# Kernel tuning notes

Measured on AMD Instinct MI355X. Metric: run time of the kernel, lower is better.

The kernel has to match this reference:

```python
import jax, jax.numpy as jnp
import numpy as np


def _lstm(x, h, c, Wih, Whh, b):
    # torch.nn.LSTMCell gate order: input, forget, cell(g), output
    g = x @ Wih + h @ Whh + b
    i, f, gg, o = jnp.split(g, 4, axis=-1)
    c = jax.nn.sigmoid(f) * c + jax.nn.sigmoid(i) * jnp.tanh(gg)
    h = jax.nn.sigmoid(o) * jnp.tanh(c)
    return h, c


def _forward(memory, mel_target, memory_lengths, prenet_W1, prenet_W2, query_W,
             memory_W, weight_vec, loc_conv_W, loc_dense_W, att_Wih, att_Whh, att_b,
             dec_Wih, dec_Whh, dec_b, proj_W, proj_b, gate_W, gate_b):
    B, n_mels, T_mel = mel_target.shape
    T_enc, enc_dim = memory.shape[1], memory.shape[2]
    att_rnn, dec_rnn = att_Whh.shape[0], dec_Whh.shape[0]
    # decoder inputs: zero frame + teacher-forced mels, one per step -> [T_mel, B, n_mels]
    dec_in = jnp.concatenate(
        [jnp.zeros((1, B, n_mels), memory.dtype), jnp.transpose(mel_target, (2, 0, 1))], 0)[:T_mel]
    # PreNet (dropout disabled: eval mode, torch uses train=self.training)
    pre = jax.nn.relu(jax.nn.relu(dec_in @ prenet_W1) @ prenet_W2)  # [T_mel, B, 256]
    processed_memory = memory @ memory_W                             # [B, T_enc, att_dim]
    valid = jnp.arange(T_enc)[None, :] < memory_lengths[:, None]     # [B, T_enc]
    pad = (loc_conv_W.shape[-1] - 1) // 2

    def step(carry, p):
        ah, ac, dh, dc, aw, awc, ctx = carry
        # attention RNN
        ah, ac = _lstm(jnp.concatenate([p, ctx], -1), ah, ac, att_Wih, att_Whh, att_b)
        # location features: conv over [prev_weights, cum_weights]
        awcat = jnp.stack([aw, awc], 1)                              # [B, 2, T_enc]
        loc = jax.lax.conv_general_dilated(awcat, loc_conv_W, (1,), [(pad, pad)],
                                           dimension_numbers=('NCH', 'OIH', 'NCH'))
        loc = jnp.einsum('bft,fa->bta', loc, loc_dense_W)            # [B, T_enc, att_dim]
        # energies and attention
        q = ah @ query_W                                             # [B, att_dim]
        e = jnp.einsum('bta,a->bt', jnp.tanh(q[:, None, :] + processed_memory + loc), weight_vec)
        e = jnp.where(valid, e, -jnp.inf)
        aw = jax.nn.softmax(e, axis=-1)                              # [B, T_enc]
        ctx = jnp.einsum('bt,btd->bd', aw, memory)                   # [B, enc_dim]
        awc = awc + aw
        # decoder RNN + projections
        dh, dc = _lstm(jnp.concatenate([ah, ctx], -1), dh, dc, dec_Wih, dec_Whh, dec_b)
        do = jnp.concatenate([dh, ctx], -1)
        mel = do @ proj_W + proj_b                                   # [B, n_mels]
        gate = (do @ gate_W + gate_b)[:, 0]                          # [B]
        return (ah, ac, dh, dc, aw, awc, ctx), (mel, gate, aw)

    z = lambda d: jnp.zeros((B, d), memory.dtype)
    carry0 = (z(att_rnn), z(att_rnn), z(dec_rnn), z(dec_rnn),
              jnp.zeros((B, T_enc), memory.dtype), jnp.zeros((B, T_enc), memory.dtype), z(enc_dim))
    _, (mels, gates, aligns) = jax.lax.scan(jax.checkpoint(step), carry0, pre)
    return (jnp.transpose(mels, (1, 2, 0)),   # [B, n_mels, T_mel]
            jnp.transpose(gates, (1, 0)),     # [B, T_mel]
            jnp.transpose(aligns, (1, 0, 2)))  # [B, T_mel, T_enc]


def setup_inputs() -> dict:
    key = jax.random.key(0)
    ks = jax.random.split(key, 20)
    B, T_enc, T_mel = 32, 400, 400
    n_mels, pre, att_rnn, dec_rnn, enc_dim, att_dim, nf, ksz = 80, 256, 1024, 1024, 512, 128, 32, 31
    rn = lambda k, s, sc=0.02: (jax.random.normal(k, s, jnp.float32) * sc)
    return dict(
        memory=jax.random.normal(ks[0], (B, T_enc, enc_dim), jnp.float32),
        mel_target=jax.random.normal(ks[1], (B, n_mels, T_mel), jnp.float32),
        memory_lengths=jax.random.randint(ks[2], (B,), T_enc // 2, T_enc + 1),
        prenet_W1=rn(ks[3], (n_mels, pre), 0.05),
        prenet_W2=rn(ks[4], (pre, pre), 0.05),
        query_W=rn(ks[5], (att_rnn, att_dim)),
        memory_W=rn(ks[6], (enc_dim, att_dim)),
        weight_vec=rn(ks[7], (att_dim,), 0.1),
        loc_conv_W=rn(ks[8], (nf, 2, ksz), 0.1),
        loc_dense_W=rn(ks[9], (nf, att_dim), 0.1),
        att_Wih=rn(ks[10], (pre + enc_dim, 4 * att_rnn)),
        att_Whh=rn(ks[11], (att_rnn, 4 * att_rnn)),
        att_b=jnp.zeros((4 * att_rnn,), jnp.float32),
        dec_Wih=rn(ks[12], (att_rnn + enc_dim, 4 * dec_rnn)),
        dec_Whh=rn(ks[13], (dec_rnn, 4 * dec_rnn)),
        dec_b=jnp.zeros((4 * dec_rnn,), jnp.float32),
        proj_W=rn(ks[14], (dec_rnn + enc_dim, n_mels)),
        proj_b=jnp.zeros((n_mels,), jnp.float32),
        gate_W=rn(ks[15], (dec_rnn + enc_dim, 1)),
        gate_b=jnp.zeros((1,), jnp.float32),
    )


def reference(memory, mel_target, memory_lengths, prenet_W1, prenet_W2, query_W,
              memory_W, weight_vec, loc_conv_W, loc_dense_W, att_Wih, att_Whh, att_b,
              dec_Wih, dec_Whh, dec_b, proj_W, proj_b, gate_W, gate_b):
    return _forward(memory, mel_target, memory_lengths, prenet_W1, prenet_W2, query_W,
                    memory_W, weight_vec, loc_conv_W, loc_dense_W, att_Wih, att_Whh, att_b,
                    dec_Wih, dec_Whh, dec_b, proj_W, proj_b, gate_W, gate_b)
```

## Files before the change

kernel.cpp:

```cpp
#include <hip/hip_runtime.h>

#define OFF_PRE   0u
#define OFF_PMT   3276800u
#define OFF_GATT  4915200u
#define OFF_GDEC  7012352u
#define OFF_E     9109504u
#define OFF_AH    9122304u
#define OFF_AC0   9155072u
#define OFF_AC1   9187840u
#define OFF_DH    9220608u
#define OFF_DC    9253376u
#define OFF_AW0   9286144u
#define OFF_AW1   9298944u
#define OFF_AWC0  9311744u
#define OFF_AWC1  9324544u
#define OFF_CTX0  9337344u
#define OFF_CTX1  9353728u
#define WS_TOTAL  9370112u

__device__ __forceinline__ float sigm(float x){ return 1.f/(1.f+__expf(-x)); }
__device__ __forceinline__ float ftanh(float x){
  x = fminf(fmaxf(x,-15.f),15.f);
  float e = __expf(2.f*x);
  return (e-1.f)/(e+1.f);
}

typedef const __attribute__((address_space(1))) unsigned int* gas_t;
typedef __attribute__((address_space(3))) unsigned int* las_t;


__global__ void zero_kernel(float* p, unsigned n){
  unsigned i = blockIdx.x*256u + threadIdx.x;
  if (i<n) p[i]=0.f;
}

__global__ __launch_bounds__(256) void prenet_kernel(const float* __restrict__ mel_target,
    const float* __restrict__ W1, const float* __restrict__ W2, float* __restrict__ pre)
{
  __shared__ float din[80];
  __shared__ float h1[256];
  int blk = blockIdx.x;
  int t = blk >> 5, b = blk & 31;
  int tid = threadIdx.x;
  if (tid < 80) din[tid] = (t==0) ? 0.f : mel_target[b*32000 + tid*400 + (t-1)];
  __syncthreads();
  float s=0.f;
  for (int c=0;c<80;c++) s += din[c]*W1[c*256+tid];
  h1[tid] = fmaxf(s,0.f);
  __syncthreads();
  float s2=0.f;
  for (int c=0;c<256;c++) s2 += h1[c]*W2[c*256+tid];
  pre[(size_t)blk*256 + tid] = fmaxf(s2,0.f);
}

__global__ __launch_bounds__(128) void pm_kernel(const float* __restrict__ memory,
    const float* __restrict__ memory_W, float* __restrict__ pmT)
{
  __shared__ float mrow[512];
  int blk = blockIdx.x;
  int b = blk/400, t = blk - b*400;
  int tid = threadIdx.x;
  const float* src = memory + (size_t)blk*512;
  for (int i=tid;i<512;i+=128) mrow[i]=src[i];
  __syncthreads();
  float s=0.f;
  for (int d=0; d<512; d++) s += mrow[d]*memory_W[d*128+tid];
  pmT[(size_t)b*51200 + tid*400 + t] = s;
}

template<int SLICE, int KIH>
__global__ __launch_bounds__(512) void gates_v3(
    const float* __restrict__ x0, int n0,
    const float* __restrict__ x1, int n1,
    const float* __restrict__ x2, int n2,
    const float* __restrict__ Wih, const float* __restrict__ Whh,
    float* __restrict__ Gp)
{
  constexpr int NT = SLICE/16;
  __shared__ float xs[SLICE*33];
  __shared__ float wbuf[3*2048];
  const int tid = threadIdx.x;
  const int k_beg = blockIdx.y * SLICE;
  const int n01 = n0 + n1;

  for (int base=0; base<32*SLICE; base+=512){
    int idx = base + tid;
    if (idx < 32*SLICE){
      int r = idx / SLICE, kk = idx - r*SLICE;
      int k = k_beg + kk;
      float v;
      if (k < n0) v = x0[r*n0 + k];
      else if (k < n01) v = x1[r*n1 + (k-n0)];
      else v = x2[r*n2 + (k-n01)];
      xs[kk*33 + r] = v;
    }
  }
  __syncthreads();

  const int wv = tid >> 6, lane = tid & 63;
  const int fb = wv*1024 + lane*16;
  const int kk_l = fb >> 9;
  const int inner = fb & 511;
  const size_t colbB = (size_t)blockIdx.x*512;

  auto STAGE = [&](int s){
    int k = k_beg + s*16 + kk_l;
    const char* row = (k < KIH) ? ((const char*)Wih + (size_t)k*16384)
                                : ((const char*)Whh + (size_t)(k-KIH)*16384);
    const char* g = row + colbB + inner;
    float* l = &wbuf[(s%3)*2048 + wv*256];
    __builtin_amdgcn_global_load_lds((gas_t)g, (las_t)l, 16, 0, 0);
  };

  STAGE(0);
  STAGE(1);

  const int rg = tid >> 5, cg = tid & 31;
  const int r0 = rg*2;
  float4 a0 = {0,0,0,0}, a1 = {0,0,0,0};

  for (int s=0; s<NT; s++){
    asm volatile("s_barrier" ::: "memory");
    if (s+2 < NT) STAGE(s+2);
    int rem = NT-1-s;
    if (rem >= 2)      asm volatile("s_waitcnt vmcnt(2)" ::: "memory");
    else if (rem == 1) asm volatile("s_waitcnt vmcnt(1)" ::: "memory");
    else               asm volatile("s_waitcnt vmcnt(0)" ::: "memory");
    asm volatile("s_barrier" ::: "memory");
    const float* wb = &wbuf[(s%3)*2048];
    const float* xk = &xs[(s*16)*33];
    #pragma unroll
    for (int kk=0; kk<16; kk++){
      float4 w = *(const float4*)(wb + kk*128 + cg*4);
      float xv0 = xk[kk*33 + r0], xv1 = xk[kk*33 + r0 + 1];
      a0.x += xv0*w.x; a0.y += xv0*w.y; a0.z += xv0*w.z; a0.w += xv0*w.w;
      a1.x += xv1*w.x; a1.y += xv1*w.y; a1.z += xv1*w.z; a1.w += xv1*w.w;
    }
  }
  float* gp = Gp + (size_t)blockIdx.y*131072 + blockIdx.x*128 + cg*4;
  *(float4*)(gp + (size_t)(r0  )*4096) = a0;
  *(float4*)(gp + (size_t)(r0+1)*4096) = a1;
}

__global__ __launch_bounds__(512) void att_mid_kernel(
    const float* __restrict__ Gp, const float* __restrict__ att_b,
    float* __restrict__ AH, const float* __restrict__ ACr, float* __restrict__ ACw,
    const float* __restrict__ query_W,
    const float* __restrict__ wc, const float* __restrict__ wd,
    const float* __restrict__ vvec, const float* __restrict__ pmT,
    const int* __restrict__ mlen,
    const float* __restrict__ AWr, const float* __restrict__ AWCr,
    float* __restrict__ E,
    const float* __restrict__ Gd, const float* __restrict__ dec_b,
    float* __restrict__ DH, float* __restrict__ DC,
    int step)
{
  __shared__ float aw_s[400], awc_s[400];
  __shared__ float wc_s[1984];
  __shared__ float wd_s[4096];
  __shared__ float v_s[128], q_s[128];
  __shared__ float ah_s[1024];
  __shared__ float pool[4608];
  const int b = blockIdx.x, yD = blockIdx.y, tid = threadIdx.x;

  for (int i=tid;i<400;i+=512){ aw_s[i]=AWr[b*400+i]; awc_s[i]=AWCr[b*400+i]; }
  for (int i=tid;i<4096;i+=512) wd_s[i]=wd[i];
  for (int i=tid;i<1984;i+=512) wc_s[i]=wc[i];
  if (tid<128) v_s[tid]=vvec[tid];

  {
    float4* g4 = (float4*)pool;
    for (int i=tid; i<1024; i+=512){
      float4 s = {0,0,0,0};
      #pragma unroll
      for (int sl=0; sl<16; sl++){
        const float4* gs = (const float4*)(Gp + (size_t)sl*131072 + (size_t)b*4096);
        float4 v = gs[i];
        s.x+=v.x; s.y+=v.y; s.z+=v.z; s.w+=v.w;
      }
      g4[i] = s;
    }
  }
  __syncthreads();
  for (int u0=0; u0<2; u0++){
    int u = tid + u0*512;
    float gi=pool[u]+att_b[u], gf=pool[1024+u]+att_b[1024+u];
    float gg=pool[2048+u]+att_b[2048+u], go=pool[3072+u]+att_b[3072+u];
    float c = sigm(gf)*ACr[b*1024+u] + sigm(gi)*ftanh(gg);
    float h = sigm(go)*ftanh(c);
    ah_s[u]=h;
    if (yD==0){ ACw[b*1024+u]=c; AH[b*1024+u]=h; }
  }
  __syncthreads();
  { int a = tid & 127, sl = tid >> 7;
    float s=0.f; int kb = sl*256;
    for (int k=kb;k<kb+256;k++) s += ah_s[k]*query_W[k*128+a];
    pool[sl*128+a]=s; }
  __syncthreads();
  if (tid<128) q_s[tid] = pool[tid]+pool[128+tid]+pool[256+tid]+pool[384+tid];
  if (step>0 && tid<128){
    int u = yD*128 + tid;
    float gi=dec_b[u], gf=dec_b[1024+u], gg=dec_b[2048+u], go=dec_b[3072+u];
    #pragma unroll
    for (int sl=0; sl<16; sl++){
      const float* g = Gd + (size_t)sl*131072 + (size_t)b*4096;
      gi+=g[u]; gf+=g[1024+u]; gg+=g[2048+u]; go+=g[3072+u];
    }
    float c = sigm(gf)*DC[b*1024+u] + sigm(gi)*ftanh(gg);
    float h = sigm(go)*ftanh(c);
    DC[b*1024+u]=c; DH[b*1024+u]=h;
  }
  __syncthreads();
  const int t0 = yD*50;
  float* loc = pool + 512;
  { int tl = tid & 63, fs = tid >> 6;
    if (tl < 50){
      float cf0=0,cf1=0,cf2=0,cf3=0;
      int f0 = fs*4;
      int tg = t0 + tl;
      for (int k=0;k<31;k++){
        int gi2 = tg + k - 15;
        float a1 = (gi2>=0 && gi2<400) ? aw_s[gi2] : 0.f;
        float a2 = (gi2>=0 && gi2<400) ? awc_s[gi2] : 0.f;
        cf0 += wc_s[(f0+0)*62+k]*a1 + wc_s[(f0+0)*62+31+k]*a2;
        cf1 += wc_s[(f0+1)*62+k]*a1 + wc_s[(f0+1)*62+31+k]*a2;
        cf2 += wc_s[(f0+2)*62+k]*a1 + wc_s[(f0+2)*62+31+k]*a2;
        cf3 += wc_s[(f0+3)*62+k]*a1 + wc_s[(f0+3)*62+31+k]*a2;
      }
      loc[tl*33+f0+0]=cf0; loc[tl*33+f0+1]=cf1;
      loc[tl*33+f0+2]=cf2; loc[tl*33+f0+3]=cf3;
    }
  }
  __syncthreads();
  float* ep = pool + 2176;
  { int tl = tid & 63, as = tid >> 6;
    if (tl < 50){
      int tg = t0 + tl;
      float e = 0.f;
      const float* lrow = loc + tl*33;
      for (int aa=0; aa<16; aa++){
        int a = as*16 + aa;
        float pmv = pmT[(size_t)b*51200 + (size_t)a*400 + tg];
        float lv = 0.f;
        #pragma unroll
        for (int f=0; f<32; f++) lv += lrow[f]*wd_s[f*128+a];
        e += ftanh(q_s[a]+pmv+lv)*v_s[a];
      }
      ep[as*64+tl] = e;
    }
  }
  __syncthreads();
  if (tid < 50){
    int tg = t0 + tid;
    float ee=0.f;
    #pragma unroll
    for (int as2=0; as2<8; as2++) ee += ep[as2*64+tid];
    E[b*400+tg] = (tg < mlen[b]) ? ee : -1e30f;
  }
}

__global__ __launch_bounds__(512) void softmax_ctx_kernel(
    const float* __restrict__ E, const float* __restrict__ memory,
    float* __restrict__ AWw, const float* __restrict__ AWCr, float* __restrict__ AWCw,
    float* __restrict__ CTXw, const float* __restrict__ CTXpp,
    const float* __restrict__ DH,
    const float* __restrict__ proj_W, const float* __restrict__ proj_b,
    const float* __restrict__ gate_W, const float* __restrict__ gate_b,
    float* __restrict__ out, float* __restrict__ aligns, int step)
{
  __shared__ float e_s[400];
  __shared__ float red[16];
  __shared__ float cp[512];
  __shared__ float do_s[1536];
  __shared__ float pps[486];
  const int b = blockIdx.x, yD = blockIdx.y, tid = threadIdx.x;

  float ev = (tid<400) ? E[b*400+tid] : -1e30f;
  float m = ev;
  for (int off=32; off>0; off>>=1) m = fmaxf(m, __shfl_down(m, off, 64));
  if ((tid&63)==0) red[tid>>6]=m;
  __syncthreads();
  if (tid==0){ float mm=red[0]; for (int i=1;i<8;i++) mm=fmaxf(mm,red[i]); red[8]=mm; }
  __syncthreads();
  m = red[8];
  float ex = (tid<400) ? __expf(ev-m) : 0.f;
  float ss = ex;
  for (int off=32; off>0; off>>=1) ss += __shfl_down(ss, off, 64);
  if ((tid&63)==0) red[tid>>6]=ss;
  __syncthreads();
  if (tid==0){ float s2=0.f; for (int i=0;i<8;i++) s2+=red[i]; red[9]=1.f/s2; }
  __syncthreads();
  float anew = ex*red[9];
  if (tid<400) e_s[tid]=anew;
  if (yD==0 && tid<400){
    AWw[b*400+tid] = anew;
    AWCw[b*400+tid] = AWCr[b*400+tid] + anew;
    aligns[(size_t)b*160000 + (size_t)step*400 + tid] = anew;
  }
  __syncthreads();
  { int d = tid & 63, ts = tid >> 6;
    const int d0 = yD*64;
    const float* mrow = memory + (size_t)b*204800 + d0 + d;
    float pacc=0.f;
    for (int tt=ts*50; tt<ts*50+50; tt++) pacc += e_s[tt]*mrow[(size_t)tt*512];
    cp[ts*64+d]=pacc; }
  __syncthreads();
  if (tid<64){
    float s2=0.f;
    #pragma unroll
    for (int ts2=0; ts2<8; ts2++) s2+=cp[ts2*64+tid];
    CTXw[b*512 + yD*64 + tid]=s2;
  }
  if (yD==0 && step>0){
    for (int i=tid; i<1536; i+=512)
      do_s[i] = (i<1024) ? DH[b*1024+i] : CTXpp[b*512 + (i-1024)];
    __syncthreads();
    int sl = tid/81, o = tid - sl*81;
    if (sl < 6){
      float s=0.f; int kb = sl*256;
      for (int k=kb;k<kb+256;k++){
        float w2 = (o<80) ? proj_W[k*80+o] : gate_W[k];
        s += do_s[k]*w2;
      }
      pps[sl*81+o]=s;
    }
    __syncthreads();
    if (tid<81){
      float r=0.f;
      #pragma unroll
      for (int s2=0;s2<6;s2++) r += pps[s2*81+tid];
      if (tid<80) out[(size_t)b*32000 + tid*400 + (step-1)] = r + proj_b[tid];
      else        out[1024000 + b*400 + (step-1)] = r + gate_b[0];
    }
  }
}

__global__ __launch_bounds__(512) void dec_final_kernel(
    const float* __restrict__ Gd, const float* __restrict__ dec_b,
    const float* __restrict__ DC, const float* __restrict__ CTX1,
    const float* __restrict__ proj_W, const float* __restrict__ proj_b,
    const float* __restrict__ gate_W, const float* __restrict__ gate_b,
    float* __restrict__ out)
{
  __shared__ float g_s[4096];
  __shared__ float do_s[1536];
  __shared__ float pps[486];
  const int b = blockIdx.x, tid = threadIdx.x;
  { float4* g4 = (float4*)g_s;
    for (int i=tid; i<1024; i+=512){
      float4 s={0,0,0,0};
      #pragma unroll
      for (int sl=0; sl<16; sl++){
        const float4* gs = (const float4*)(Gd + (size_t)sl*131072 + (size_t)b*4096);
        float4 v = gs[i];
        s.x+=v.x; s.y+=v.y; s.z+=v.z; s.w+=v.w;
      }
      g4[i]=s;
    } }
  __syncthreads();
  for (int u0=0; u0<2; u0++){
    int u = tid + u0*512;
    float gi=g_s[u]+dec_b[u], gf=g_s[1024+u]+dec_b[1024+u];
    float gg=g_s[2048+u]+dec_b[2048+u], go=g_s[3072+u]+dec_b[3072+u];
    float c = sigm(gf)*DC[b*1024+u] + sigm(gi)*ftanh(gg);
    do_s[u] = sigm(go)*ftanh(c);
  }
  if (tid<512) do_s[1024+tid] = CTX1[b*512+tid];
  __syncthreads();
  int sl = tid/81, o = tid - sl*81;
  if (sl < 6){
    float s=0.f; int kb = sl*256;
    for (int k=kb;k<kb+256;k++){
      float w2 = (o<80) ? proj_W[k*80+o] : gate_W[k];
      s += do_s[k]*w2;
    }
    pps[sl*81+o]=s;
  }
  __syncthreads();
  if (tid<81){
    float r=0.f;
    #pragma unroll
    for (int s2=0;s2<6;s2++) r += pps[s2*81+tid];
    if (tid<80) out[(size_t)b*32000 + tid*400 + 399] = r + proj_b[tid];
    else        out[1024000 + b*400 + 399] = r + gate_b[0];
  }
}


extern "C" void kernel_launch(void* const* d_in, const int* in_sizes, int n_in,
                              void* d_out, int out_size, void* d_ws, size_t ws_size,
                              hipStream_t stream) {
  const float* memory      = (const float*)d_in[0];
  const float* mel_target  = (const float*)d_in[1];
  const int*   mlen        = (const int*)  d_in[2];
  const float* prenet_W1   = (const float*)d_in[3];
  const float* prenet_W2   = (const float*)d_in[4];
  const float* query_W     = (const float*)d_in[5];
  const float* memory_W    = (const float*)d_in[6];
  const float* weight_vec  = (const float*)d_in[7];
  const float* loc_conv_W  = (const float*)d_in[8];
  const float* loc_dense_W = (const float*)d_in[9];
  const float* att_Wih     = (const float*)d_in[10];
  const float* att_Whh     = (const float*)d_in[11];
  const float* att_b       = (const float*)d_in[12];
  const float* dec_Wih     = (const float*)d_in[13];
  const float* dec_Whh     = (const float*)d_in[14];
  const float* dec_b       = (const float*)d_in[15];
  const float* proj_W      = (const float*)d_in[16];
  const float* proj_b      = (const float*)d_in[17];
  const float* gate_W      = (const float*)d_in[18];
  const float* gate_b      = (const float*)d_in[19];
  float* out = (float*)d_out;
  float* ws  = (float*)d_ws;

  float* PRE  = ws + OFF_PRE;
  float* PMT  = ws + OFF_PMT;
  float* GATT = ws + OFF_GATT;
  float* GDEC = ws + OFF_GDEC;
  float* E    = ws + OFF_E;
  float* AH   = ws + OFF_AH;
  float* AC[2] = { ws + OFF_AC0, ws + OFF_AC1 };
  float* DH   = ws + OFF_DH;
  float* DC   = ws + OFF_DC;
  float* AW[2] = { ws + OFF_AW0, ws + OFF_AW1 };
  float* AWC[2]= { ws + OFF_AWC0, ws + OFF_AWC1 };
  float* CTX[2]= { ws + OFF_CTX0, ws + OFF_CTX1 };
  float* aligns = out + 1036800;

  hipLaunchKernelGGL(zero_kernel, dim3((WS_TOTAL+255u)/256u), dim3(256), 0, stream, ws, WS_TOTAL);
  hipLaunchKernelGGL(prenet_kernel, dim3(12800), dim3(256), 0, stream,
                     mel_target, prenet_W1, prenet_W2, PRE);
  hipLaunchKernelGGL(pm_kernel, dim3(12800), dim3(128), 0, stream, memory, memory_W, PMT);

  for (int t=0; t<400; t++){
    const int p = t & 1, pp = 1 - p;
    hipLaunchKernelGGL((gates_v3<112,768>), dim3(32,16), dim3(512), 0, stream,
        PRE + (size_t)t*8192, 256, CTX[pp], 512, AH, 1024,
        att_Wih, att_Whh, GATT);
    hipLaunchKernelGGL(att_mid_kernel, dim3(32,8), dim3(512), 0, stream,
        GATT, att_b, AH, AC[pp], AC[p], query_W, loc_conv_W, loc_dense_W,
        weight_vec, PMT, mlen, AW[pp], AWC[pp], E,
        GDEC, dec_b, DH, DC, t);
    hipLaunchKernelGGL(softmax_ctx_kernel, dim3(32,8), dim3(512), 0, stream,
        E, memory, AW[p], AWC[pp], AWC[p], CTX[p], CTX[pp],
        DH, proj_W, proj_b, gate_W, gate_b, out, aligns, t);
    hipLaunchKernelGGL((gates_v3<160,1536>), dim3(32,16), dim3(512), 0, stream,
        AH, 1024, CTX[p], 512, DH, 1024,
        dec_Wih, dec_Whh, GDEC);
  }
  hipLaunchKernelGGL(dec_final_kernel, dim3(32), dim3(512), 0, stream,
      GDEC, dec_b, DC, CTX[1], proj_W, proj_b, gate_W, gate_b, out);
}
```

Before: 71.90 ms.

## Fuse per-step decoder kernels into one persistent cooperative kernel with grid barriers

Replaces the 1600 per-step kernel launches with a single cooperative persistent kernel of 256 blocks that runs all 400 decoder steps, separating phases with an atomic-counter grid barrier. The gates matmul split-K count drops from 16 to 8 slices (larger slices), so the partial-sum buffers and reductions shrink. Weight staging in the gates phase moves from triple to double buffering, and x loads become float2. This removes launch overhead and inter-kernel gaps but adds spin-barrier costs and reduces parallelism per phase.

```diff
diff --git a/kernel.cpp b/kernel.cpp
--- a/kernel.cpp
+++ b/kernel.cpp
@@ -1,22 +1,28 @@
 #include <hip/hip_runtime.h>
+
+#define NBLK 256
+#define NTHR 512
 
 #define OFF_PRE   0u
 #define OFF_PMT   3276800u
 #define OFF_GATT  4915200u
-#define OFF_GDEC  7012352u
-#define OFF_E     9109504u
-#define OFF_AH    9122304u
-#define OFF_AC0   9155072u
-#define OFF_AC1   9187840u
-#define OFF_DH    9220608u
-#define OFF_DC    9253376u
-#define OFF_AW0   9286144u
-#define OFF_AW1   9298944u
-#define OFF_AWC0  9311744u
-#define OFF_AWC1  9324544u
-#define OFF_CTX0  9337344u
-#define OFF_CTX1  9353728u
-#define WS_TOTAL  9370112u
+#define OFF_GDEC  5963776u
+#define OFF_E     7012352u
+#define OFF_AH    7025152u
+#define OFF_AC0   7057920u
+#define OFF_AC1   7090688u
+#define OFF_DH    7123456u
+#define OFF_DC    7156224u
+#define OFF_AW0   7188992u
+#define OFF_AW1   7201792u
+#define OFF_AWC0  7214592u
+#define OFF_AWC1  7227392u
+#define OFF_CTX0  7240192u
+#define OFF_CTX1  7256576u
+#define OFF_BAR   7272960u
+#define WS_TOTAL  7272976u
+
+#define LDS_FLOATS 14976
 
 __device__ __forceinline__ float sigm(float x){ return 1.f/(1.f+__expf(-x)); }
 __device__ __forceinline__ float ftanh(float x){
@@ -27,6 +33,24 @@
 
 typedef const __attribute__((address_space(1))) unsigned int* gas_t;
 typedef __attribute__((address_space(3))) unsigned int* las_t;
+
+__device__ __forceinline__ void gsync(unsigned* bar){
+  __syncthreads();
+  if (threadIdx.x==0){
+    __threadfence();
+    unsigned g = __hip_atomic_load(bar+1, __ATOMIC_ACQUIRE, __HIP_MEMORY_SCOPE_AGENT);
+    unsigned arrived = __hip_atomic_fetch_add(bar, 1u, __ATOMIC_ACQ_REL, __HIP_MEMORY_SCOPE_AGENT);
+    if (arrived == NBLK-1u){
+      __hip_atomic_store(bar, 0u, __ATOMIC_RELAXED, __HIP_MEMORY_SCOPE_AGENT);
+      __hip_atomic_fetch_add(bar+1, 1u, __ATOMIC_ACQ_REL, __HIP_MEMORY_SCOPE_AGENT);
+    } else {
+      while (__hip_atomic_load(bar+1, __ATOMIC_ACQUIRE, __HIP_MEMORY_SCOPE_AGENT) == g){
+        __builtin_amdgcn_s_sleep(2);
+      }
+    }
+  }
+  __syncthreads();
+}
 
 
 __global__ void zero_kernel(float* p, unsigned n){
@@ -69,111 +93,105 @@
 }
 
 template<int SLICE, int KIH>
-__global__ __launch_bounds__(512) void gates_v3(
-    const float* __restrict__ x0, int n0,
-    const float* __restrict__ x1, int n1,
-    const float* __restrict__ x2, int n2,
-    const float* __restrict__ Wih, const float* __restrict__ Whh,
-    float* __restrict__ Gp)
+__device__ __forceinline__ void gates_phase(
+    float* sm,
+    const float* x0, int n0, const float* x1, int n1, const float* x2, int n2,
+    const float* Wih, const float* Whh, float* Gp)
 {
   constexpr int NT = SLICE/16;
-  __shared__ float xs[SLICE*33];
-  __shared__ float wbuf[3*2048];
+  float* xs = sm;
+  float* wbuf = sm + SLICE*34;
   const int tid = threadIdx.x;
-  const int k_beg = blockIdx.y * SLICE;
-  const int n01 = n0 + n1;
-
-  for (int base=0; base<32*SLICE; base+=512){
-    int idx = base + tid;
+  const int bid = blockIdx.x;
+  const int cb = bid & 31;
+  const int kh = bid >> 5;
+  const int k_beg = kh*SLICE;
+  const int n01 = n0+n1;
+  for (int base=0; base<32*SLICE; base+=NTHR){
+    int idx = base+tid;
     if (idx < 32*SLICE){
-      int r = idx / SLICE, kk = idx - r*SLICE;
+      int r = idx/SLICE, kk = idx - r*SLICE;
       int k = k_beg + kk;
       float v;
-      if (k < n0) v = x0[r*n0 + k];
-      else if (k < n01) v = x1[r*n1 + (k-n0)];
-      else v = x2[r*n2 + (k-n01)];
-      xs[kk*33 + r] = v;
-    }
-  }
-  __syncthreads();
-
-  const int wv = tid >> 6, lane = tid & 63;
+      if (k<n0) v = x0[r*n0+k];
+      else if (k<n01) v = x1[r*n1+(k-n0)];
+      else v = x2[r*n2+(k-n01)];
+      xs[kk*34+r] = v;
+    }
+  }
+  __syncthreads();
+  const int wv = tid>>6, lane = tid&63;
   const int fb = wv*1024 + lane*16;
-  const int kk_l = fb >> 9;
+  const int kk_l = fb>>9;
   const int inner = fb & 511;
-  const size_t colbB = (size_t)blockIdx.x*512;
+  const size_t colbB = (size_t)cb*512;
 
   auto STAGE = [&](int s){
     int k = k_beg + s*16 + kk_l;
-    const char* row = (k < KIH) ? ((const char*)Wih + (size_t)k*16384)
-                                : ((const char*)Whh + (size_t)(k-KIH)*16384);
+    const char* row = (k<KIH) ? ((const char*)Wih + (size_t)k*16384)
+                              : ((const char*)Whh + (size_t)(k-KIH)*16384);
     const char* g = row + colbB + inner;
-    float* l = &wbuf[(s%3)*2048 + wv*256];
+    float* l = &wbuf[(s&1)*2048 + wv*256];
     __builtin_amdgcn_global_load_lds((gas_t)g, (las_t)l, 16, 0, 0);
   };
-
   STAGE(0);
-  STAGE(1);
-
-  const int rg = tid >> 5, cg = tid & 31;
+  const int rg = tid>>5, cg = tid&31;
   const int r0 = rg*2;
-  float4 a0 = {0,0,0,0}, a1 = {0,0,0,0};
-
+  float4 a0={0,0,0,0}, a1={0,0,0,0};
   for (int s=0; s<NT; s++){
+    if (s+1<NT){
+      STAGE(s+1);
+      asm volatile("s_waitcnt vmcnt(1)" ::: "memory");
+    } else {
+      asm volatile("s_waitcnt vmcnt(0)" ::: "memory");
+    }
     asm volatile("s_barrier" ::: "memory");
-    if (s+2 < NT) STAGE(s+2);
-    int rem = NT-1-s;
-    if (rem >= 2)      asm volatile("s_waitcnt vmcnt(2)" ::: "memory");
-    else if (rem == 1) asm volatile("s_waitcnt vmcnt(1)" ::: "memory");
-    else               asm volatile("s_waitcnt vmcnt(0)" ::: "memory");
-    asm volatile("s_barrier" ::: "memory");
-    const float* wb = &wbuf[(s%3)*2048];
-    const float* xk = &xs[(s*16)*33];
+    const float* wb = wbuf + (s&1)*2048;
+    const float* xk = xs + (s*16)*34;
     #pragma unroll
     for (int kk=0; kk<16; kk++){
       float4 w = *(const float4*)(wb + kk*128 + cg*4);
-      float xv0 = xk[kk*33 + r0], xv1 = xk[kk*33 + r0 + 1];
-      a0.x += xv0*w.x; a0.y += xv0*w.y; a0.z += xv0*w.z; a0.w += xv0*w.w;
-      a1.x += xv1*w.x; a1.y += xv1*w.y; a1.z += xv1*w.z; a1.w += xv1*w.w;
-    }
-  }
-  float* gp = Gp + (size_t)blockIdx.y*131072 + blockIdx.x*128 + cg*4;
+      float2 xv = *(const float2*)(xk + kk*34 + r0);
+      a0.x += xv.x*w.x; a0.y += xv.x*w.y; a0.z += xv.x*w.z; a0.w += xv.x*w.w;
+      a1.x += xv.y*w.x; a1.y += xv.y*w.y; a1.z += xv.y*w.z; a1.w += xv.y*w.w;
+    }
+    asm volatile("s_barrier" ::: "memory");
+  }
+  float* gp = Gp + (size_t)kh*131072 + cb*128 + cg*4;
   *(float4*)(gp + (size_t)(r0  )*4096) = a0;
   *(float4*)(gp + (size_t)(r0+1)*4096) = a1;
 }
 
-__global__ __launch_bounds__(512) void att_mid_kernel(
-    const float* __restrict__ Gp, const float* __restrict__ att_b,
-    float* __restrict__ AH, const float* __restrict__ ACr, float* __restrict__ ACw,
-    const float* __restrict__ query_W,
-    const float* __restrict__ wc, const float* __restrict__ wd,
-    const float* __restrict__ vvec, const float* __restrict__ pmT,
-    const int* __restrict__ mlen,
-    const float* __restrict__ AWr, const float* __restrict__ AWCr,
-    float* __restrict__ E,
-    const float* __restrict__ Gd, const float* __restrict__ dec_b,
-    float* __restrict__ DH, float* __restrict__ DC,
-    int step)
-{
-  __shared__ float aw_s[400], awc_s[400];
-  __shared__ float wc_s[1984];
-  __shared__ float wd_s[4096];
-  __shared__ float v_s[128], q_s[128];
-  __shared__ float ah_s[1024];
-  __shared__ float pool[4608];
-  const int b = blockIdx.x, yD = blockIdx.y, tid = threadIdx.x;
-
-  for (int i=tid;i<400;i+=512){ aw_s[i]=AWr[b*400+i]; awc_s[i]=AWCr[b*400+i]; }
-  for (int i=tid;i<4096;i+=512) wd_s[i]=wd[i];
-  for (int i=tid;i<1984;i+=512) wc_s[i]=wc[i];
+__device__ __forceinline__ void att_mid_phase(
+    float* sm, const float* Gp, const float* att_b,
+    float* AH, const float* ACr, float* ACw,
+    const float* query_W, const float* wcv, const float* wdv, const float* vvec,
+    const float* pmT, const int* mlen,
+    const float* AWr, const float* AWCr, float* E,
+    const float* Gd, const float* dec_b, float* DH, float* DC, int step)
+{
+  float* ah_s = sm;
+  float* wd_s = sm+1024;
+  float* wc_s = sm+5120;
+  float* aw_s = sm+7104;
+  float* awc_s= sm+7504;
+  float* v_s  = sm+7904;
+  float* q_s  = sm+8032;
+  float* pool = sm+8160;
+  const int bid = blockIdx.x, tid = threadIdx.x;
+  const int b = bid & 31, yD = bid >> 5;
+
+  for (int i=tid;i<400;i+=NTHR){ aw_s[i]=AWr[b*400+i]; awc_s[i]=AWCr[b*400+i]; }
+  for (int i=tid;i<4096;i+=NTHR) wd_s[i]=wdv[i];
+  for (int i=tid;i<1984;i+=NTHR) wc_s[i]=wcv[i];
   if (tid<128) v_s[tid]=vvec[tid];
 
   {
     float4* g4 = (float4*)pool;
-    for (int i=tid; i<1024; i+=512){
+    for (int i=tid; i<1024; i+=NTHR){
       float4 s = {0,0,0,0};
       #pragma unroll
-      for (int sl=0; sl<16; sl++){
+      for (int sl=0; sl<8; sl++){
         const float4* gs = (const float4*)(Gp + (size_t)sl*131072 + (size_t)b*4096);
         float4 v = gs[i];
         s.x+=v.x; s.y+=v.y; s.z+=v.z; s.w+=v.w;
@@ -183,7 +201,7 @@
   }
   __syncthreads();
   for (int u0=0; u0<2; u0++){
-    int u = tid + u0*512;
+    int u = tid + u0*NTHR;
     float gi=pool[u]+att_b[u], gf=pool[1024+u]+att_b[1024+u];
     float gg=pool[2048+u]+att_b[2048+u], go=pool[3072+u]+att_b[3072+u];
     float c = sigm(gf)*ACr[b*1024+u] + sigm(gi)*ftanh(gg);
@@ -202,7 +220,7 @@
     int u = yD*128 + tid;
     float gi=dec_b[u], gf=dec_b[1024+u], gg=dec_b[2048+u], go=dec_b[3072+u];
     #pragma unroll
-    for (int sl=0; sl<16; sl++){
+    for (int sl=0; sl<8; sl++){
       const float* g = Gd + (size_t)sl*131072 + (size_t)b*4096;
       gi+=g[u]; gf+=g[1024+u]; gg+=g[2048+u]; go+=g[3072+u];
     }
@@ -259,21 +277,21 @@
   }
 }
 
-__global__ __launch_bounds__(512) void softmax_ctx_kernel(
-    const float* __restrict__ E, const float* __restrict__ memory,
-    float* __restrict__ AWw, const float* __restrict__ AWCr, float* __restrict__ AWCw,
-    float* __restrict__ CTXw, const float* __restrict__ CTXpp,
-    const float* __restrict__ DH,
-    const float* __restrict__ proj_W, const float* __restrict__ proj_b,
-    const float* __restrict__ gate_W, const float* __restrict__ gate_b,
-    float* __restrict__ out, float* __restrict__ aligns, int step)
-{
-  __shared__ float e_s[400];
-  __shared__ float red[16];
-  __shared__ float cp[512];
-  __shared__ float do_s[1536];
-  __shared__ float pps[486];
-  const int b = blockIdx.x, yD = blockIdx.y, tid = threadIdx.x;
+__device__ __forceinline__ void softmax_ctx_phase(
+    float* sm, const float* E, const float* memory,
+    float* AWw, const float* AWCr, float* AWCw,
+    float* CTXw, const float* CTXpp, const float* DH,
+    const float* proj_W, const float* proj_b,
+    const float* gate_W, const float* gate_b,
+    float* out, float* aligns, int step)
+{
+  float* e_s = sm;
+  float* red = sm+400;
+  float* cp  = sm+416;
+  float* do_s= sm+928;
+  float* pps = sm+2464;
+  const int bid = blockIdx.x, tid = threadIdx.x;
+  const int b = bid & 31, yD = bid >> 5;
 
   float ev = (tid<400) ? E[b*400+tid] : -1e30f;
   float m = ev;
@@ -312,7 +330,7 @@
     CTXw[b*512 + yD*64 + tid]=s2;
   }
   if (yD==0 && step>0){
-    for (int i=tid; i<1536; i+=512)
+    for (int i=tid; i<1536; i+=NTHR)
       do_s[i] = (i<1024) ? DH[b*1024+i] : CTXpp[b*512 + (i-1024)];
     __syncthreads();
     int sl = tid/81, o = tid - sl*81;
@@ -335,22 +353,21 @@
   }
 }
 
-__global__ __launch_bounds__(512) void dec_final_kernel(
-    const float* __restrict__ Gd, const float* __restrict__ dec_b,
-    const float* __restrict__ DC, const float* __restrict__ CTX1,
-    const float* __restrict__ proj_W, const float* __restrict__ proj_b,
-    const float* __restrict__ gate_W, const float* __restrict__ gate_b,
-    float* __restrict__ out)
-{
-  __shared__ float g_s[4096];
-  __shared__ float do_s[1536];
-  __shared__ float pps[486];
+__device__ __forceinline__ void dec_final_phase(
+    float* sm, const float* Gd, const float* dec_b,
+    const float* DC, const float* CTX1,
+    const float* proj_W, const float* proj_b,
+    const float* gate_W, const float* gate_b, float* out)
+{
+  float* g_s = sm;
+  float* do_s= sm+4096;
+  float* pps = sm+5632;
   const int b = blockIdx.x, tid = threadIdx.x;
   { float4* g4 = (float4*)g_s;
-    for (int i=tid; i<1024; i+=512){
+    for (int i=tid; i<1024; i+=NTHR){
       float4 s={0,0,0,0};
       #pragma unroll
-      for (int sl=0; sl<16; sl++){
+      for (int sl=0; sl<8; sl++){
         const float4* gs = (const float4*)(Gd + (size_t)sl*131072 + (size_t)b*4096);
         float4 v = gs[i];
         s.x+=v.x; s.y+=v.y; s.z+=v.z; s.w+=v.w;
@@ -359,13 +376,13 @@
     } }
   __syncthreads();
   for (int u0=0; u0<2; u0++){
-    int u = tid + u0*512;
+    int u = tid + u0*NTHR;
     float gi=g_s[u]+dec_b[u], gf=g_s[1024+u]+dec_b[1024+u];
     float gg=g_s[2048+u]+dec_b[2048+u], go=g_s[3072+u]+dec_b[3072+u];
     float c = sigm(gf)*DC[b*1024+u] + sigm(gi)*ftanh(gg);
     do_s[u] = sigm(go)*ftanh(c);
   }
-  if (tid<512) do_s[1024+tid] = CTX1[b*512+tid];
+  do_s[1024+tid] = CTX1[b*512+tid];
   __syncthreads();
   int sl = tid/81, o = tid - sl*81;
   if (sl < 6){
@@ -384,6 +401,50 @@
     if (tid<80) out[(size_t)b*32000 + tid*400 + 399] = r + proj_b[tid];
     else        out[1024000 + b*400 + 399] = r + gate_b[0];
   }
+}
+
+__global__ void __launch_bounds__(NTHR) decoder_persist(
+    const float* memory, const int* mlen, const float* query_W,
+    const float* wcv, const float* wdv, const float* vvec,
+    const float* att_Wih, const float* att_Whh, const float* att_b,
+    const float* dec_Wih, const float* dec_Whh, const float* dec_b,
+    const float* proj_W, const float* proj_b,
+    const float* gate_W, const float* gate_b,
+    float* ws, float* out)
+{
+  extern __shared__ float sm[];
+  float* PRE  = ws + OFF_PRE;
+  float* PMT  = ws + OFF_PMT;
+  float* GATT = ws + OFF_GATT;
+  float* GDEC = ws + OFF_GDEC;
+  float* E    = ws + OFF_E;
+  float* AH   = ws + OFF_AH;
+  float* AC_[2] = { ws + OFF_AC0, ws + OFF_AC1 };
+  float* DH   = ws + OFF_DH;
+  float* DC   = ws + OFF_DC;
+  float* AW_[2] = { ws + OFF_AW0, ws + OFF_AW1 };
+  float* AWC_[2]= { ws + OFF_AWC0, ws + OFF_AWC1 };
+  float* CTX_[2]= { ws + OFF_CTX0, ws + OFF_CTX1 };
+  unsigned* bar = (unsigned*)(ws + OFF_BAR);
+  float* aligns = out + 1036800;
+
+  for (int t=0; t<400; t++){
+    const int p = t & 1, pp = 1 - p;
+    gates_phase<224,768>(sm, PRE + (size_t)t*8192, 256, CTX_[pp], 512, AH, 1024,
+                         att_Wih, att_Whh, GATT);
+    gsync(bar);
+    att_mid_phase(sm, GATT, att_b, AH, AC_[pp], AC_[p], query_W, wcv, wdv, vvec,
+                  PMT, mlen, AW_[pp], AWC_[pp], E, GDEC, dec_b, DH, DC, t);
+    gsync(bar);
+    softmax_ctx_phase(sm, E, memory, AW_[p], AWC_[pp], AWC_[p], CTX_[p], CTX_[pp],
+                      DH, proj_W, proj_b, gate_W, gate_b, out, aligns, t);
+    gsync(bar);
+    gates_phase<320,1536>(sm, AH, 1024, CTX_[p], 512, DH, 1024,
+                          dec_Wih, dec_Whh, GDEC);
+    gsync(bar);
+  }
+  if (blockIdx.x < 32)
+    dec_final_phase(sm, GDEC, dec_b, DC, CTX_[1], proj_W, proj_b, gate_W, gate_b, out);
 }
 
 
@@ -413,41 +474,22 @@
   float* out = (float*)d_out;
   float* ws  = (float*)d_ws;
 
-  float* PRE  = ws + OFF_PRE;
-  float* PMT  = ws + OFF_PMT;
-  float* GATT = ws + OFF_GATT;
-  float* GDEC = ws + OFF_GDEC;
-  float* E    = ws + OFF_E;
-  float* AH   = ws + OFF_AH;
-  float* AC[2] = { ws + OFF_AC0, ws + OFF_AC1 };
-  float* DH   = ws + OFF_DH;
-  float* DC   = ws + OFF_DC;
-  float* AW[2] = { ws + OFF_AW0, ws + OFF_AW1 };
-  float* AWC[2]= { ws + OFF_AWC0, ws + OFF_AWC1 };
-  float* CTX[2]= { ws + OFF_CTX0, ws + OFF_CTX1 };
-  float* aligns = out + 1036800;
+  float* PRE = ws + OFF_PRE;
+  float* PMT = ws + OFF_PMT;
 
   hipLaunchKernelGGL(zero_kernel, dim3((WS_TOTAL+255u)/256u), dim3(256), 0, stream, ws, WS_TOTAL);
   hipLaunchKernelGGL(prenet_kernel, dim3(12800), dim3(256), 0, stream,
                      mel_target, prenet_W1, prenet_W2, PRE);
   hipLaunchKernelGGL(pm_kernel, dim3(12800), dim3(128), 0, stream, memory, memory_W, PMT);
 
-  for (int t=0; t<400; t++){
-    const int p = t & 1, pp = 1 - p;
-    hipLaunchKernelGGL((gates_v3<112,768>), dim3(32,16), dim3(512), 0, stream,
-        PRE + (size_t)t*8192, 256, CTX[pp], 512, AH, 1024,
-        att_Wih, att_Whh, GATT);
-    hipLaunchKernelGGL(att_mid_kernel, dim3(32,8), dim3(512), 0, stream,
-        GATT, att_b, AH, AC[pp], AC[p], query_W, loc_conv_W, loc_dense_W,
-        weight_vec, PMT, mlen, AW[pp], AWC[pp], E,
-        GDEC, dec_b, DH, DC, t);
-    hipLaunchKernelGGL(softmax_ctx_kernel, dim3(32,8), dim3(512), 0, stream,
-        E, memory, AW[p], AWC[pp], AWC[p], CTX[p], CTX[pp],
-        DH, proj_W, proj_b, gate_W, gate_b, out, aligns, t);
-    hipLaunchKernelGGL((gates_v3<160,1536>), dim3(32,16), dim3(512), 0, stream,
-        AH, 1024, CTX[p], 512, DH, 1024,
-        dec_Wih, dec_Whh, GDEC);
-  }
-  hipLaunchKernelGGL(dec_final_kernel, dim3(32), dim3(512), 0, stream,
-      GDEC, dec_b, DC, CTX[1], proj_W, proj_b, gate_W, gate_b, out);
-}
+  void* args[] = {
+    (void*)&memory, (void*)&mlen, (void*)&query_W,
+    (void*)&loc_conv_W, (void*)&loc_dense_W, (void*)&weight_vec,
+    (void*)&att_Wih, (void*)&att_Whh, (void*)&att_b,
+    (void*)&dec_Wih, (void*)&dec_Whh, (void*)&dec_b,
+    (void*)&proj_W, (void*)&proj_b, (void*)&gate_W, (void*)&gate_b,
+    (void*)&ws, (void*)&out
+  };
+  hipLaunchCooperativeKernel((const void*)decoder_persist, dim3(NBLK), dim3(NTHR),
+                             args, LDS_FLOATS*sizeof(float), stream);
+}
```

Measured after the change: 224.4 ms. +212.1%, slower.
